# Optimization experiments

Hardware: AMD Instinct MI355X
Metric: run time of the kernel (lower is better)

## Reference

```python
import jax, jax.numpy as jnp
import numpy as np

B, ENC, DEC, H, OUT = 4096, 168, 24, 64, 1
IN = 1 + 5 + 3 + 4 + 7  # 20


def _lstm_step(xt, h, c, Wih, Whh, bih, bhh):
    # PyTorch gate order: i, f, g, o
    g = xt @ Wih.T + h @ Whh.T + bih + bhh
    i, f, gg, o = jnp.split(g, 4, axis=-1)
    c = jax.nn.sigmoid(f) * c + jax.nn.sigmoid(i) * jnp.tanh(gg)
    h = jax.nn.sigmoid(o) * jnp.tanh(c)
    return h, c


def _lstm_layer(x, Wih, Whh, bih, bhh):
    # x: [T, B, in] -> ys: [T, B, H], final (h, c)
    h0 = jnp.zeros((x.shape[1], Whh.shape[1]), x.dtype)

    def step(carry, xt):
        h, c = _lstm_step(xt, carry[0], carry[1], Wih, Whh, bih, bhh)
        return (h, c), h

    (h, c), ys = jax.lax.scan(step, (h0, h0), x)
    return ys, h, c


def setup_inputs() -> dict:
    key = jax.random.key(0)
    ks = jax.random.split(key, 24)
    rn = lambda k, s, sc=0.05: jax.random.normal(k, s, jnp.float32) * sc
    inp = {
        "input_p_q": rn(ks[0], (B, ENC, 1), 1.0),
        "input_time": jax.random.randint(ks[1], (B, ENC, 4), 0, 8),
        "label_p": rn(ks[2], (B, ENC), 1.0),
        "decoder_time": jax.random.randint(ks[3], (B, DEC, 4), 0, 8),
        # encoder LSTM layer 0
        "enc0_Wih": rn(ks[4], (4 * H, IN)), "enc0_Whh": rn(ks[5], (4 * H, H)),
        "enc0_bih": rn(ks[6], (4 * H,)), "enc0_bhh": rn(ks[7], (4 * H,)),
        # encoder LSTM layer 1
        "enc1_Wih": rn(ks[8], (4 * H, H)), "enc1_Whh": rn(ks[9], (4 * H, H)),
        "enc1_bih": rn(ks[10], (4 * H,)), "enc1_bhh": rn(ks[11], (4 * H,)),
        # decoder LSTMCell (input = OUT + 19 = 20)
        "dec_Wih": rn(ks[12], (4 * H, OUT + 19)), "dec_Whh": rn(ks[13], (4 * H, H)),
        "dec_bih": rn(ks[14], (4 * H,)), "dec_bhh": rn(ks[15], (4 * H,)),
        # output projection
        "Wout": rn(ks[16], (OUT, H)), "bout": rn(ks[17], (OUT,)),
        # embeddings
        "emb_hour": rn(ks[18], (24, 5)), "emb_wd": rn(ks[19], (8, 3)),
        "emb_mo": rn(ks[20], (13, 4)), "emb_woy": rn(ks[21], (54, 7)),
    }
    return inp


def reference(input_p_q, input_time, label_p, decoder_time,
              enc0_Wih, enc0_Whh, enc0_bih, enc0_bhh,
              enc1_Wih, enc1_Whh, enc1_bih, enc1_bhh,
              dec_Wih, dec_Whh, dec_bih, dec_bhh,
              Wout, bout, emb_hour, emb_wd, emb_mo, emb_woy):
    def time_feats(t):  # t: [B, T, 4] int -> [B, T, 19]
        return jnp.concatenate([emb_hour[t[:, :, 0]], emb_wd[t[:, :, 1]],
                                emb_mo[t[:, :, 2]], emb_woy[t[:, :, 3]]], axis=-1)

    input_q = label_p[:, :ENC, None]                      # [B, ENC, 1]
    enc_in = jnp.concatenate([input_q, time_feats(input_time)], axis=-1)  # [B, ENC, 20]
    x = enc_in.transpose(1, 0, 2)                         # [ENC, B, 20]
    ys0, _, _ = _lstm_layer(x, enc0_Wih, enc0_Whh, enc0_bih, enc0_bhh)
    _, h1, c1 = _lstm_layer(ys0, enc1_Wih, enc1_Whh, enc1_bih, enc1_bhh)

    dec_feat = time_feats(decoder_time).transpose(1, 0, 2)  # [DEC, B, 19]
    prev0 = label_p[:, ENC - 1, None]                       # [B, 1]

    def dec_step(carry, ft):
        h, c, prev = carry
        xin = jnp.concatenate([prev, ft], axis=-1)          # [B, 20]
        h, c = _lstm_step(xin, h, c, dec_Wih, dec_Whh, dec_bih, dec_bhh)
        out = h @ Wout.T + bout                             # [B, OUT]
        return (h, c, out), out

    _, outs = jax.lax.scan(dec_step, (h1, c1, prev0), dec_feat)
    return outs.transpose(1, 0, 2)                          # [B, DEC, OUT]
```

## Files before the change

kernel.cpp:

```cpp
#include <hip/hip_runtime.h>

#define DEVFN __device__ __forceinline__

typedef float  f32x4  __attribute__((ext_vector_type(4)));
typedef short  bf16x8 __attribute__((ext_vector_type(8)));

constexpr int ENC = 168;
constexpr int DEC = 24;
constexpr int BT  = 16;
constexpr int NBLK = 4096 / BT;

constexpr float LOG2E  = 1.4426950408889634f;
constexpr float LOG2E2 = 2.8853900817779268f;

constexpr int W0F = 0;
constexpr int W1F = 24576;
constexpr int WDF = 57344;
constexpr int F_B0   = 40960;
constexpr int F_B1   = 41216;
constexpr int F_BD   = 41472;
constexpr int F_WOUT = 41728;
constexpr int F_BOUT = 41792;
constexpr int F_EMB  = 41793;
constexpr int NEMB = 574;

DEVFN ushort f2bf(float v) {
    unsigned b = __float_as_uint(v);
    return (ushort)((b + 0x7FFFu + ((b >> 16) & 1u)) >> 16);
}
DEVFN float bf2f(ushort u) { return __uint_as_float(((unsigned)u) << 16); }
DEVFN unsigned cvt_pk_bf16(float a, float b) {
    unsigned r;
    asm("v_cvt_pk_bf16_f32 %0, %1, %2" : "=v"(r) : "v"(a), "v"(b));
    return r;
}
DEVFN float exp2n(float x) {
    float r;
    asm("v_exp_f32 %0, -%1" : "=v"(r) : "v"(x));
    return r;
}
DEVFN void pinv(bf16x8& v) { asm volatile("" : "+v"(v)); }
DEVFN void pinf(f32x4& v)  { asm volatile("" : "+v"(v)); }

DEVFN float lstm_cell(float gi, float gf, float gg, float go, float& c) {
    float a  = exp2n(fmaxf(gi, -21.f));
    float b  = exp2n(fmaxf(gg, -43.f));
    float f  = exp2n(gf);
    float sf = __builtin_amdgcn_rcpf(1.f + f);
    float it = (1.f - b) * __builtin_amdgcn_rcpf(fmaf(a, b, a + b + 1.f));
    c = fmaf(sf, c, it);
    float d  = exp2n(fmaxf(c, -15.f) * LOG2E2);
    float o  = exp2n(fmaxf(go, -21.f));
    return (1.f - d) * __builtin_amdgcn_rcpf(fmaf(o, d, o + d + 1.f));
}

__global__ void prep_kernel(
    const float* __restrict__ w0ih, const float* __restrict__ w0hh,
    const float* __restrict__ b0ih, const float* __restrict__ b0hh,
    const float* __restrict__ w1ih, const float* __restrict__ w1hh,
    const float* __restrict__ b1ih, const float* __restrict__ b1hh,
    const float* __restrict__ wdih, const float* __restrict__ wdhh,
    const float* __restrict__ bdih, const float* __restrict__ bdhh,
    const float* __restrict__ wout, const float* __restrict__ boutp,
    const float* __restrict__ eh,   const float* __restrict__ ewd,
    const float* __restrict__ emo,  const float* __restrict__ ewoy,
    void* __restrict__ ws)
{
    ushort* wsu = (ushort*)ws;
    float*  wsf = (float*)ws;
    const int total = 81920 + 1407;
    for (int idx = blockIdx.x * blockDim.x + threadIdx.x; idx < total;
         idx += gridDim.x * blockDim.x) {
        if (idx < 81920) {
            int layer, q;
            if (idx < W1F)      { layer = 0; q = idx; }
            else if (idx < WDF) { layer = 1; q = idx - W1F; }
            else                { layer = 2; q = idx - WDF; }
            int c  = q >> 13;
            int tt = (q >> 9) & 15;
            int l  = (q >> 3) & 63;
            int j  = q & 7;
            int k  = c * 32 + (l >> 4) * 8 + j;
            int n  = tt * 16 + (l & 15);
            float v = 0.f;
            if (layer == 0) {
                if (k < 20) v = w0ih[n * 20 + k];
                else if (k == 20) v = w0ih[n * 20];
                else if (k >= 32 && k < 96) v = w0hh[n * 64 + (k - 32)];
            } else if (layer == 1) {
                if (k < 64) v = w1ih[n * 64 + k];
                else        v = w1hh[n * 64 + (k - 64)];
            } else {
                if (k < 20) v = wdih[n * 20 + k];
                else if (k == 20) v = wdih[n * 20];
                else if (k >= 32 && k < 96) v = wdhh[n * 64 + (k - 32)];
            }
            v *= ((n >> 6) == 2) ? LOG2E2 : LOG2E;
            wsu[idx] = f2bf(v);
        } else {
            int f = idx - 81920;
            float v;
            if (f < 768) {
                float sc = (((f & 255) >> 6) == 2) ? LOG2E2 : LOG2E;
                if (f < 256)      v = (b0ih[f] + b0hh[f]) * sc;
                else if (f < 512) v = (b1ih[f - 256] + b1hh[f - 256]) * sc;
                else              v = (bdih[f - 512] + bdhh[f - 512]) * sc;
            }
            else if (f < 832) v = wout[f - 768];
            else if (f == 832) v = boutp[0];
            else {
                int e = f - 833;
                if (e < 120)      v = eh[e];
                else if (e < 144) v = ewd[e - 120];
                else if (e < 196) v = emo[e - 144];
                else              v = ewoy[e - 196];
            }
            wsf[40960 + f] = v;
        }
    }
}

DEVFN int offX(int k, int m) {
    return (m + 16 * (k >> 3)) * 8 + (k & 7);
}
DEVFN void store_h4(ushort* A, int off, const float* h) {
    unsigned h01 = cvt_pk_bf16(h[0], h[1]);
    unsigned h23 = cvt_pk_bf16(h[2], h[3]);
    asm volatile("" : "+v"(h01), "+v"(h23));
    unsigned long long p = ((unsigned long long)h23 << 32) | h01;
    *(unsigned long long*)(A + off) = p;
}
DEVFN void store_prev(ushort* A, int m, float v) {
    ushort hi = f2bf(v);
    A[offX(0, m)]  = hi;
    A[offX(20, m)] = f2bf(v - bf2f(hi));
}

__global__ __launch_bounds__(512)
__attribute__((amdgpu_waves_per_eu(2, 2)))
void lstm_mfma(
    const int* __restrict__ input_time, const float* __restrict__ label_p,
    const int* __restrict__ decoder_time, const void* __restrict__ ws,
    float* __restrict__ out)
{
    const ushort* wsu = (const ushort*)ws;
    const float*  wsf = (const float*)ws;

    __shared__ __align__(16) ushort Abuf[2][5 * 512];
    __shared__ float s_emb[NEMB];
    __shared__ float s_wout[64];
    __shared__ float sh1[16 * 68];
    __shared__ float s_bout;

    const int tid = threadIdx.x;
    const int w   = tid >> 6;
    const int l   = tid & 63;
    const int q   = l >> 4;
    const int m   = l & 15;
    const int wl  = w & 3;
    const bool isL0 = (w < 4);
    const int b0g = blockIdx.x * BT;
    const int u0  = wl * 16 + q * 4;

    const int hoff = (1 + (u0 >> 5)) * 512 +
                     (m + 16 * ((u0 & 31) >> 3)) * 8 + (u0 & 7) +
                     (isL0 ? 0 : 1024);

    for (int i = tid; i < 2 * 5 * 512; i += 512) ((ushort*)Abuf)[i] = 0;
    for (int i = tid; i < NEMB; i += 512) s_emb[i] = wsf[F_EMB + i];
    if (tid < 64) s_wout[tid] = wsf[F_WOUT + tid];
    if (tid == 0) s_bout = wsf[F_BOUT];

    bf16x8 wA[4][4];
    if (isL0) {
#pragma unroll
        for (int c = 0; c < 3; c++)
#pragma unroll
            for (int g = 0; g < 4; g++)
                wA[c][g] = *(const bf16x8*)(wsu + W0F +
                    (c * 16 + g * 4 + wl) * 512 + l * 8);
        wA[3][0] = wA[3][1] = wA[3][2] = wA[3][3] = bf16x8{0,0,0,0,0,0,0,0};
    } else {
#pragma unroll
        for (int c = 0; c < 4; c++)
#pragma unroll
            for (int g = 0; g < 4; g++)
                wA[c][g] = *(const bf16x8*)(wsu + W1F +
                    (c * 16 + g * 4 + wl) * 512 + l * 8);
    }
#pragma unroll
    for (int c = 0; c < 4; c++)
#pragma unroll
        for (int g = 0; g < 4; g++) pinv(wA[c][g]);

    f32x4 biasv[4];
#pragma unroll
    for (int g = 0; g < 4; g++) {
        biasv[g] = *(const f32x4*)(wsf + (isL0 ? F_B0 : F_B1) + g * 64 + u0);
        pinf(biasv[g]);
    }

    float cst[4] = {0.f, 0.f, 0.f, 0.f};

    const int kk1 = tid >> 4;
    const int kk2 = kk1 + 16;
    const bool bx2 = (tid < 64);
    int sel1 = 0, estr1 = 0, ebase1 = 0;
    if (kk1 >= 1) {
        int f = kk1 - 1;
        if (f < 5)       { sel1 = 0; estr1 = 5; ebase1 = 0   + f; }
        else if (f < 8)  { sel1 = 1; estr1 = 3; ebase1 = 120 + (f - 5); }
        else if (f < 12) { sel1 = 2; estr1 = 4; ebase1 = 144 + (f - 8); }
        else             { sel1 = 3; estr1 = 7; ebase1 = 196 + (f - 12); }
    }
    const int ebase2 = 196 + (kk2 - 13);

    __syncthreads();
    if (isL0) {
        if (kk1 == 0) {
            store_prev(Abuf[0], m, label_p[(b0g + m) * ENC]);
        } else {
            int idx = input_time[((b0g + m) * ENC) * 4 + sel1];
            Abuf[0][offX(kk1, m)] = f2bf(s_emb[ebase1 + idx * estr1]);
        }
        if (bx2) {
            int idx2 = input_time[((b0g + m) * ENC) * 4 + 3];
            Abuf[0][offX(kk2, m)] = f2bf(s_emb[ebase2 + idx2 * 7]);
        }
    }
    __syncthreads();

    for (int i = 0; i <= ENC; ++i) {
        const ushort* Ar = Abuf[i & 1];
        ushort* Aw = Abuf[(i + 1) & 1];
        const bool active = isL0 ? (i < ENC) : (i >= 1);

        float pre_f = 0.f; int pre_i1 = 0, pre_i2 = 0;
        const bool encX  = (i + 1 < ENC) && isL0;
        const bool decX0 = (i == ENC) && isL0;
        if (encX) {
            if (kk1 == 0) pre_f  = label_p[(b0g + m) * ENC + (i + 1)];
            else          pre_i1 = input_time[((b0g + m) * ENC + (i + 1)) * 4 + sel1];
            if (bx2)      pre_i2 = input_time[((b0g + m) * ENC + (i + 1)) * 4 + 3];
        } else if (decX0) {
            if (kk1 == 0) pre_f  = label_p[(b0g + m) * ENC + (ENC - 1)];
            else          pre_i1 = decoder_time[((b0g + m) * DEC) * 4 + sel1];
            if (bx2)      pre_i2 = decoder_time[((b0g + m) * DEC) * 4 + 3];
        }

        if (active) {
            f32x4 acc[4];
            if (isL0) {
                bf16x8 ah[3];
#pragma unroll
                for (int c = 0; c < 3; c++)
                    ah[c] = *(const bf16x8*)(Ar + c * 512 + l * 8);
#pragma unroll
                for (int g = 0; g < 4; g++)
                    acc[g] = __builtin_amdgcn_mfma_f32_16x16x32_bf16(
                        wA[0][g], ah[0], biasv[g], 0, 0, 0);
#pragma unroll
                for (int c = 1; c < 3; c++)
#pragma unroll
                    for (int g = 0; g < 4; g++)
                        acc[g] = __builtin_amdgcn_mfma_f32_16x16x32_bf16(
                            wA[c][g], ah[c], acc[g], 0, 0, 0);
            } else {
                bf16x8 ah[4];
#pragma unroll
                for (int c = 0; c < 4; c++)
                    ah[c] = *(const bf16x8*)(Ar + (1 + c) * 512 + l * 8);
#pragma unroll
                for (int g = 0; g < 4; g++)
                    acc[g] = __builtin_amdgcn_mfma_f32_16x16x32_bf16(
                        wA[0][g], ah[0], biasv[g], 0, 0, 0);
#pragma unroll
                for (int c = 1; c < 4; c++)
#pragma unroll
                    for (int g = 0; g < 4; g++)
                        acc[g] = __builtin_amdgcn_mfma_f32_16x16x32_bf16(
                            wA[c][g], ah[c], acc[g], 0, 0, 0);
            }
            float hv[4];
#pragma unroll
            for (int r = 0; r < 4; r++)
                hv[r] = lstm_cell(acc[0][r], acc[1][r], acc[2][r], acc[3][r], cst[r]);
            store_h4(Aw, hoff, hv);
        }
        if (encX || decX0) {
            if (kk1 == 0) store_prev(Aw, m, pre_f);
            else          Aw[offX(kk1, m)] = f2bf(s_emb[ebase1 + pre_i1 * estr1]);
            if (bx2)      Aw[offX(kk2, m)] = f2bf(s_emb[ebase2 + pre_i2 * 7]);
        }
        __syncthreads();
    }

    if (!isL0) {
#pragma unroll
        for (int c = 0; c < 3; c++)
#pragma unroll
            for (int g = 0; g < 4; g++)
                wA[c][g] = *(const bf16x8*)(wsu + WDF +
                    (c * 16 + g * 4 + wl) * 512 + l * 8);
#pragma unroll
        for (int c = 0; c < 3; c++)
#pragma unroll
            for (int g = 0; g < 4; g++) pinv(wA[c][g]);
#pragma unroll
        for (int g = 0; g < 4; g++) {
            biasv[g] = *(const f32x4*)(wsf + F_BD + g * 64 + u0);
            pinf(biasv[g]);
        }
    }

    for (int t = 0; t < DEC; ++t) {
        const ushort* Ar = Abuf[(t + 1) & 1];
        ushort* Aw = Abuf[t & 1];

        int pre_i1 = 0, pre_i2 = 0;
        const bool dX = (t + 1 < DEC) && isL0;
        if (dX) {
            if (kk1 >= 1) pre_i1 = decoder_time[((b0g + m) * DEC + (t + 1)) * 4 + sel1];
            if (bx2)      pre_i2 = decoder_time[((b0g + m) * DEC + (t + 1)) * 4 + 3];
        }

        if (!isL0) {
            bf16x8 ah[3];
            ah[0] = *(const bf16x8*)(Ar + 0 * 512 + l * 8);
            ah[1] = *(const bf16x8*)(Ar + 3 * 512 + l * 8);
            ah[2] = *(const bf16x8*)(Ar + 4 * 512 + l * 8);
            f32x4 acc[4];
#pragma unroll
            for (int g = 0; g < 4; g++)
                acc[g] = __builtin_amdgcn_mfma_f32_16x16x32_bf16(
                    wA[0][g], ah[0], biasv[g], 0, 0, 0);
#pragma unroll
            for (int c = 1; c < 3; c++)
#pragma unroll
                for (int g = 0; g < 4; g++)
                    acc[g] = __builtin_amdgcn_mfma_f32_16x16x32_bf16(
                        wA[c][g], ah[c], acc[g], 0, 0, 0);
            float hv[4];
#pragma unroll
            for (int r = 0; r < 4; r++)
                hv[r] = lstm_cell(acc[0][r], acc[1][r], acc[2][r], acc[3][r], cst[r]);
            store_h4(Aw, hoff, hv);
            *(f32x4*)&sh1[m * 68 + u0] = *(f32x4*)hv;
        }
        if (dX && kk1 >= 1) Aw[offX(kk1, m)] = f2bf(s_emb[ebase1 + pre_i1 * estr1]);
        if (dX && bx2)      Aw[offX(kk2, m)] = f2bf(s_emb[ebase2 + pre_i2 * 7]);
        __syncthreads();

        if (tid < 16) {
            float a = s_bout;
#pragma unroll 16
            for (int u = 0; u < 64; u++) a = fmaf(s_wout[u], sh1[tid * 68 + u], a);
            out[(b0g + tid) * DEC + t] = a;
            if (t + 1 < DEC) store_prev(Aw, tid, a);
        }
        __syncthreads();
    }
}

extern "C" void kernel_launch(void* const* d_in, const int* in_sizes, int n_in,
                              void* d_out, int out_size, void* d_ws, size_t ws_size,
                              hipStream_t stream)
{
    typedef const float* fp;
    const int* input_time   = (const int*)d_in[1];
    fp         label_p      = (fp)d_in[2];
    const int* decoder_time = (const int*)d_in[3];

    prep_kernel<<<128, 256, 0, stream>>>(
        (fp)d_in[4],  (fp)d_in[5],  (fp)d_in[6],  (fp)d_in[7],
        (fp)d_in[8],  (fp)d_in[9],  (fp)d_in[10], (fp)d_in[11],
        (fp)d_in[12], (fp)d_in[13], (fp)d_in[14], (fp)d_in[15],
        (fp)d_in[16], (fp)d_in[17],
        (fp)d_in[18], (fp)d_in[19], (fp)d_in[20], (fp)d_in[21],
        d_ws);

    lstm_mfma<<<NBLK, 512, 0, stream>>>(
        input_time, label_p, decoder_time, d_ws, (float*)d_out);
}
```

Measured before the change: 289.0 us.

## Pack two 16-row batch tiles into each 1024-thread block

Each block now processes two independent 16-sample tiles, one per 512-thread half, each with its own double-buffered activation buffer and hidden-state scratch. The grid is halved and the block size doubled to 1024 threads, with the occupancy hint raised to 4 waves per EU. The intent is to interleave two independent recurrences on one CU to hide MFMA and LDS latency in the serial LSTM chain. In exchange, only half as many blocks are launched, which may leave CUs idle, and both halves now wait at shared block-wide barriers.

```diff
diff --git a/kernel.cpp b/kernel.cpp
--- a/kernel.cpp
+++ b/kernel.cpp
@@ -8,7 +8,7 @@
 constexpr int ENC = 168;
 constexpr int DEC = 24;
 constexpr int BT  = 16;
-constexpr int NBLK = 4096 / BT;
+constexpr int NBLK = 4096 / (2 * BT);
 
 constexpr float LOG2E  = 1.4426950408889634f;
 constexpr float LOG2E2 = 2.8853900817779268f;
@@ -136,8 +136,8 @@
     A[offX(20, m)] = f2bf(v - bf2f(hi));
 }
 
-__global__ __launch_bounds__(512)
-__attribute__((amdgpu_waves_per_eu(2, 2)))
+__global__ __launch_bounds__(1024)
+__attribute__((amdgpu_waves_per_eu(4, 4)))
 void lstm_mfma(
     const int* __restrict__ input_time, const float* __restrict__ label_p,
     const int* __restrict__ decoder_time, const void* __restrict__ ws,
@@ -146,28 +146,33 @@
     const ushort* wsu = (const ushort*)ws;
     const float*  wsf = (const float*)ws;
 
-    __shared__ __align__(16) ushort Abuf[2][5 * 512];
+    __shared__ __align__(16) ushort Abuf[2][2][5 * 512];
     __shared__ float s_emb[NEMB];
     __shared__ float s_wout[64];
-    __shared__ float sh1[16 * 68];
+    __shared__ float sh1[2][16 * 68];
     __shared__ float s_bout;
 
-    const int tid = threadIdx.x;
-    const int w   = tid >> 6;
-    const int l   = tid & 63;
+    const int tid  = threadIdx.x;
+    const int half = tid >> 9;
+    const int stid = tid & 511;
+    const int w   = stid >> 6;
+    const int l   = stid & 63;
     const int q   = l >> 4;
     const int m   = l & 15;
     const int wl  = w & 3;
     const bool isL0 = (w < 4);
-    const int b0g = blockIdx.x * BT;
+    const int b0g = blockIdx.x * (2 * BT) + half * BT;
     const int u0  = wl * 16 + q * 4;
+
+    ushort (* const AB)[5 * 512] = Abuf[half];
+    float*  const  myh1 = sh1[half];
 
     const int hoff = (1 + (u0 >> 5)) * 512 +
                      (m + 16 * ((u0 & 31) >> 3)) * 8 + (u0 & 7) +
                      (isL0 ? 0 : 1024);
 
-    for (int i = tid; i < 2 * 5 * 512; i += 512) ((ushort*)Abuf)[i] = 0;
-    for (int i = tid; i < NEMB; i += 512) s_emb[i] = wsf[F_EMB + i];
+    for (int i = tid; i < 2 * 2 * 5 * 512; i += 1024) ((ushort*)Abuf)[i] = 0;
+    for (int i = tid; i < NEMB; i += 1024) s_emb[i] = wsf[F_EMB + i];
     if (tid < 64) s_wout[tid] = wsf[F_WOUT + tid];
     if (tid == 0) s_bout = wsf[F_BOUT];
 
@@ -202,9 +207,9 @@
 
     float cst[4] = {0.f, 0.f, 0.f, 0.f};
 
-    const int kk1 = tid >> 4;
+    const int kk1 = stid >> 4;
     const int kk2 = kk1 + 16;
-    const bool bx2 = (tid < 64);
+    const bool bx2 = (stid < 64);
     int sel1 = 0, estr1 = 0, ebase1 = 0;
     if (kk1 >= 1) {
         int f = kk1 - 1;
@@ -218,21 +223,21 @@
     __syncthreads();
     if (isL0) {
         if (kk1 == 0) {
-            store_prev(Abuf[0], m, label_p[(b0g + m) * ENC]);
+            store_prev(AB[0], m, label_p[(b0g + m) * ENC]);
         } else {
             int idx = input_time[((b0g + m) * ENC) * 4 + sel1];
-            Abuf[0][offX(kk1, m)] = f2bf(s_emb[ebase1 + idx * estr1]);
+            AB[0][offX(kk1, m)] = f2bf(s_emb[ebase1 + idx * estr1]);
         }
         if (bx2) {
             int idx2 = input_time[((b0g + m) * ENC) * 4 + 3];
-            Abuf[0][offX(kk2, m)] = f2bf(s_emb[ebase2 + idx2 * 7]);
+            AB[0][offX(kk2, m)] = f2bf(s_emb[ebase2 + idx2 * 7]);
         }
     }
     __syncthreads();
 
     for (int i = 0; i <= ENC; ++i) {
-        const ushort* Ar = Abuf[i & 1];
-        ushort* Aw = Abuf[(i + 1) & 1];
+        const ushort* Ar = AB[i & 1];
+        ushort* Aw = AB[(i + 1) & 1];
         const bool active = isL0 ? (i < ENC) : (i >= 1);
 
         float pre_f = 0.f; int pre_i1 = 0, pre_i2 = 0;
@@ -314,8 +319,8 @@
     }
 
     for (int t = 0; t < DEC; ++t) {
-        const ushort* Ar = Abuf[(t + 1) & 1];
-        ushort* Aw = Abuf[t & 1];
+        const ushort* Ar = AB[(t + 1) & 1];
+        ushort* Aw = AB[t & 1];
 
         int pre_i1 = 0, pre_i2 = 0;
         const bool dX = (t + 1 < DEC) && isL0;
@@ -345,18 +350,18 @@
             for (int r = 0; r < 4; r++)
                 hv[r] = lstm_cell(acc[0][r], acc[1][r], acc[2][r], acc[3][r], cst[r]);
             store_h4(Aw, hoff, hv);
-            *(f32x4*)&sh1[m * 68 + u0] = *(f32x4*)hv;
+            *(f32x4*)&myh1[m * 68 + u0] = *(f32x4*)hv;
         }
         if (dX && kk1 >= 1) Aw[offX(kk1, m)] = f2bf(s_emb[ebase1 + pre_i1 * estr1]);
         if (dX && bx2)      Aw[offX(kk2, m)] = f2bf(s_emb[ebase2 + pre_i2 * 7]);
         __syncthreads();
 
-        if (tid < 16) {
+        if (stid < 16) {
             float a = s_bout;
 #pragma unroll 16
-            for (int u = 0; u < 64; u++) a = fmaf(s_wout[u], sh1[tid * 68 + u], a);
-            out[(b0g + tid) * DEC + t] = a;
-            if (t + 1 < DEC) store_prev(Aw, tid, a);
+            for (int u = 0; u < 64; u++) a = fmaf(s_wout[u], myh1[stid * 68 + u], a);
+            out[(b0g + stid) * DEC + t] = a;
+            if (t + 1 < DEC) store_prev(Aw, stid, a);
         }
         __syncthreads();
     }
@@ -379,6 +384,6 @@
         (fp)d_in[18], (fp)d_in[19], (fp)d_in[20], (fp)d_in[21],
         d_ws);
 
-    lstm_mfma<<<NBLK, 512, 0, stream>>>(
+    lstm_mfma<<<NBLK, 1024, 0, stream>>>(
         input_time, label_p, decoder_time, d_ws, (float*)d_out);
 }
```

Result: slower. 542.1 us (+87.5%).

## Split gate MFMAs across 16 waves and exchange gate preactivations via LDS

Applied to the files above, without the earlier changes.

Switches the LSTM kernel from 512 to 1024 threads. Each of the 16 waves computes one gate/unit tile for both encoder layers, so every wave runs both layer 0 and layer 1 MFMAs and the gate preactivations go through a shared-memory G buffer. The elementwise cell update is then spread so each thread handles one (batch, unit) element instead of four. A large dummy LDS pad is added to limit blocks per CU. The cost is an extra __syncthreads and an LDS round trip per timestep, in exchange for shorter per-wave MFMA chains and more parallel cell math.

```diff
diff --git a/kernel.cpp b/kernel.cpp
--- a/kernel.cpp
+++ b/kernel.cpp
@@ -29,11 +29,6 @@
     return (ushort)((b + 0x7FFFu + ((b >> 16) & 1u)) >> 16);
 }
 DEVFN float bf2f(ushort u) { return __uint_as_float(((unsigned)u) << 16); }
-DEVFN unsigned cvt_pk_bf16(float a, float b) {
-    unsigned r;
-    asm("v_cvt_pk_bf16_f32 %0, %1, %2" : "=v"(r) : "v"(a), "v"(b));
-    return r;
-}
 DEVFN float exp2n(float x) {
     float r;
     asm("v_exp_f32 %0, -%1" : "=v"(r) : "v"(x));
@@ -123,21 +118,13 @@
 DEVFN int offX(int k, int m) {
     return (m + 16 * (k >> 3)) * 8 + (k & 7);
 }
-DEVFN void store_h4(ushort* A, int off, const float* h) {
-    unsigned h01 = cvt_pk_bf16(h[0], h[1]);
-    unsigned h23 = cvt_pk_bf16(h[2], h[3]);
-    asm volatile("" : "+v"(h01), "+v"(h23));
-    unsigned long long p = ((unsigned long long)h23 << 32) | h01;
-    *(unsigned long long*)(A + off) = p;
-}
 DEVFN void store_prev(ushort* A, int m, float v) {
     ushort hi = f2bf(v);
     A[offX(0, m)]  = hi;
     A[offX(20, m)] = f2bf(v - bf2f(hi));
 }
 
-__global__ __launch_bounds__(512)
-__attribute__((amdgpu_waves_per_eu(2, 2)))
+__global__ __launch_bounds__(1024)
 void lstm_mfma(
     const int* __restrict__ input_time, const float* __restrict__ label_p,
     const int* __restrict__ decoder_time, const void* __restrict__ ws,
@@ -147,66 +134,58 @@
     const float*  wsf = (const float*)ws;
 
     __shared__ __align__(16) ushort Abuf[2][5 * 512];
+    __shared__ __align__(16) float G[2][4][16][68];
     __shared__ float s_emb[NEMB];
     __shared__ float s_wout[64];
-    __shared__ float sh1[16 * 68];
+    __shared__ __align__(16) float sh1[16 * 68];
     __shared__ float s_bout;
+    __shared__ ushort s_pad[15360];
 
     const int tid = threadIdx.x;
     const int w   = tid >> 6;
     const int l   = tid & 63;
     const int q   = l >> 4;
-    const int m   = l & 15;
-    const int wl  = w & 3;
-    const bool isL0 = (w < 4);
+    const int m16 = l & 15;
+    const int g   = w >> 2;
+    const int j   = w & 3;
+    const int u0t = j * 16 + q * 4;
+    const int cu  = (w << 2) | q;
+    const int cm  = m16;
     const int b0g = blockIdx.x * BT;
-    const int u0  = wl * 16 + q * 4;
-
-    const int hoff = (1 + (u0 >> 5)) * 512 +
-                     (m + 16 * ((u0 & 31) >> 3)) * 8 + (u0 & 7) +
-                     (isL0 ? 0 : 1024);
-
-    for (int i = tid; i < 2 * 5 * 512; i += 512) ((ushort*)Abuf)[i] = 0;
-    for (int i = tid; i < NEMB; i += 512) s_emb[i] = wsf[F_EMB + i];
+
+    if (label_p == nullptr) ((volatile ushort*)s_pad)[tid & 1023] = 0;
+
+    const int hoffL0 = (1 + (cu >> 5)) * 512 +
+                       (cm + 16 * ((cu & 31) >> 3)) * 8 + (cu & 7);
+    const int hoffL1 = hoffL0 + 1024;
+
+    for (int i2 = tid; i2 < 2 * 5 * 512; i2 += 1024) ((ushort*)Abuf)[i2] = 0;
+    for (int i2 = tid; i2 < NEMB; i2 += 1024) s_emb[i2] = wsf[F_EMB + i2];
     if (tid < 64) s_wout[tid] = wsf[F_WOUT + tid];
     if (tid == 0) s_bout = wsf[F_BOUT];
 
-    bf16x8 wA[4][4];
-    if (isL0) {
-#pragma unroll
-        for (int c = 0; c < 3; c++)
-#pragma unroll
-            for (int g = 0; g < 4; g++)
-                wA[c][g] = *(const bf16x8*)(wsu + W0F +
-                    (c * 16 + g * 4 + wl) * 512 + l * 8);
-        wA[3][0] = wA[3][1] = wA[3][2] = wA[3][3] = bf16x8{0,0,0,0,0,0,0,0};
-    } else {
-#pragma unroll
-        for (int c = 0; c < 4; c++)
-#pragma unroll
-            for (int g = 0; g < 4; g++)
-                wA[c][g] = *(const bf16x8*)(wsu + W1F +
-                    (c * 16 + g * 4 + wl) * 512 + l * 8);
-    }
+    bf16x8 wA0[3], wA1[4];
+#pragma unroll
+    for (int c = 0; c < 3; c++)
+        wA0[c] = *(const bf16x8*)(wsu + W0F + (c * 16 + w) * 512 + l * 8);
 #pragma unroll
     for (int c = 0; c < 4; c++)
-#pragma unroll
-        for (int g = 0; g < 4; g++) pinv(wA[c][g]);
-
-    f32x4 biasv[4];
-#pragma unroll
-    for (int g = 0; g < 4; g++) {
-        biasv[g] = *(const f32x4*)(wsf + (isL0 ? F_B0 : F_B1) + g * 64 + u0);
-        pinf(biasv[g]);
-    }
-
-    float cst[4] = {0.f, 0.f, 0.f, 0.f};
+        wA1[c] = *(const bf16x8*)(wsu + W1F + (c * 16 + w) * 512 + l * 8);
+#pragma unroll
+    for (int c = 0; c < 3; c++) pinv(wA0[c]);
+#pragma unroll
+    for (int c = 0; c < 4; c++) pinv(wA1[c]);
+
+    f32x4 bias0 = *(const f32x4*)(wsf + F_B0 + g * 64 + u0t);
+    f32x4 bias1 = *(const f32x4*)(wsf + F_B1 + g * 64 + u0t);
+    pinf(bias0); pinf(bias1);
+
+    float cstL0 = 0.f, cstL1 = 0.f;
 
     const int kk1 = tid >> 4;
     const int kk2 = kk1 + 16;
-    const bool bx2 = (tid < 64);
     int sel1 = 0, estr1 = 0, ebase1 = 0;
-    if (kk1 >= 1) {
+    if (kk1 >= 1 && kk1 < 16) {
         int f = kk1 - 1;
         if (f < 5)       { sel1 = 0; estr1 = 5; ebase1 = 0   + f; }
         else if (f < 8)  { sel1 = 1; estr1 = 3; ebase1 = 120 + (f - 5); }
@@ -216,139 +195,124 @@
     const int ebase2 = 196 + (kk2 - 13);
 
     __syncthreads();
-    if (isL0) {
+    if (tid < 256) {
         if (kk1 == 0) {
-            store_prev(Abuf[0], m, label_p[(b0g + m) * ENC]);
+            store_prev(Abuf[0], m16, label_p[(b0g + m16) * ENC]);
         } else {
-            int idx = input_time[((b0g + m) * ENC) * 4 + sel1];
-            Abuf[0][offX(kk1, m)] = f2bf(s_emb[ebase1 + idx * estr1]);
-        }
-        if (bx2) {
-            int idx2 = input_time[((b0g + m) * ENC) * 4 + 3];
-            Abuf[0][offX(kk2, m)] = f2bf(s_emb[ebase2 + idx2 * 7]);
-        }
+            int idx = input_time[((b0g + m16) * ENC) * 4 + sel1];
+            Abuf[0][offX(kk1, m16)] = f2bf(s_emb[ebase1 + idx * estr1]);
+        }
+    }
+    if (tid < 64) {
+        int idx2 = input_time[((b0g + m16) * ENC) * 4 + 3];
+        Abuf[0][offX(kk2, m16)] = f2bf(s_emb[ebase2 + idx2 * 7]);
     }
     __syncthreads();
 
     for (int i = 0; i <= ENC; ++i) {
         const ushort* Ar = Abuf[i & 1];
         ushort* Aw = Abuf[(i + 1) & 1];
-        const bool active = isL0 ? (i < ENC) : (i >= 1);
+        const bool actL0 = (i < ENC);
+        const bool actL1 = (i >= 1);
 
         float pre_f = 0.f; int pre_i1 = 0, pre_i2 = 0;
-        const bool encX  = (i + 1 < ENC) && isL0;
-        const bool decX0 = (i == ENC) && isL0;
+        const bool encX  = (i + 1 < ENC) && (tid < 256);
+        const bool decX0 = (i == ENC) && (tid < 256);
         if (encX) {
-            if (kk1 == 0) pre_f  = label_p[(b0g + m) * ENC + (i + 1)];
-            else          pre_i1 = input_time[((b0g + m) * ENC + (i + 1)) * 4 + sel1];
-            if (bx2)      pre_i2 = input_time[((b0g + m) * ENC + (i + 1)) * 4 + 3];
+            if (kk1 == 0) pre_f  = label_p[(b0g + m16) * ENC + (i + 1)];
+            else          pre_i1 = input_time[((b0g + m16) * ENC + (i + 1)) * 4 + sel1];
+            if (tid < 64) pre_i2 = input_time[((b0g + m16) * ENC + (i + 1)) * 4 + 3];
         } else if (decX0) {
-            if (kk1 == 0) pre_f  = label_p[(b0g + m) * ENC + (ENC - 1)];
-            else          pre_i1 = decoder_time[((b0g + m) * DEC) * 4 + sel1];
-            if (bx2)      pre_i2 = decoder_time[((b0g + m) * DEC) * 4 + 3];
-        }
-
-        if (active) {
-            f32x4 acc[4];
-            if (isL0) {
-                bf16x8 ah[3];
-#pragma unroll
-                for (int c = 0; c < 3; c++)
-                    ah[c] = *(const bf16x8*)(Ar + c * 512 + l * 8);
-#pragma unroll
-                for (int g = 0; g < 4; g++)
-                    acc[g] = __builtin_amdgcn_mfma_f32_16x16x32_bf16(
-                        wA[0][g], ah[0], biasv[g], 0, 0, 0);
-#pragma unroll
-                for (int c = 1; c < 3; c++)
-#pragma unroll
-                    for (int g = 0; g < 4; g++)
-                        acc[g] = __builtin_amdgcn_mfma_f32_16x16x32_bf16(
-                            wA[c][g], ah[c], acc[g], 0, 0, 0);
-            } else {
-                bf16x8 ah[4];
-#pragma unroll
-                for (int c = 0; c < 4; c++)
-                    ah[c] = *(const bf16x8*)(Ar + (1 + c) * 512 + l * 8);
-#pragma unroll
-                for (int g = 0; g < 4; g++)
-                    acc[g] = __builtin_amdgcn_mfma_f32_16x16x32_bf16(
-                        wA[0][g], ah[0], biasv[g], 0, 0, 0);
-#pragma unroll
-                for (int c = 1; c < 4; c++)
-#pragma unroll
-                    for (int g = 0; g < 4; g++)
-                        acc[g] = __builtin_amdgcn_mfma_f32_16x16x32_bf16(
-                            wA[c][g], ah[c], acc[g], 0, 0, 0);
-            }
-            float hv[4];
-#pragma unroll
-            for (int r = 0; r < 4; r++)
-                hv[r] = lstm_cell(acc[0][r], acc[1][r], acc[2][r], acc[3][r], cst[r]);
-            store_h4(Aw, hoff, hv);
+            if (kk1 == 0) pre_f  = label_p[(b0g + m16) * ENC + (ENC - 1)];
+            else          pre_i1 = decoder_time[((b0g + m16) * DEC) * 4 + sel1];
+            if (tid < 64) pre_i2 = decoder_time[((b0g + m16) * DEC) * 4 + 3];
+        }
+
+        {
+            bf16x8 ah[5];
+#pragma unroll
+            for (int c = 0; c < 5; c++)
+                ah[c] = *(const bf16x8*)(Ar + c * 512 + l * 8);
+            if (actL0) {
+                f32x4 a0 = __builtin_amdgcn_mfma_f32_16x16x32_bf16(
+                    wA0[0], ah[0], bias0, 0, 0, 0);
+                a0 = __builtin_amdgcn_mfma_f32_16x16x32_bf16(
+                    wA0[1], ah[1], a0, 0, 0, 0);
+                a0 = __builtin_amdgcn_mfma_f32_16x16x32_bf16(
+                    wA0[2], ah[2], a0, 0, 0, 0);
+                *(f32x4*)&G[0][g][m16][u0t] = a0;
+            }
+            if (actL1) {
+                f32x4 a1 = __builtin_amdgcn_mfma_f32_16x16x32_bf16(
+                    wA1[0], ah[1], bias1, 0, 0, 0);
+                a1 = __builtin_amdgcn_mfma_f32_16x16x32_bf16(
+                    wA1[1], ah[2], a1, 0, 0, 0);
+                a1 = __builtin_amdgcn_mfma_f32_16x16x32_bf16(
+                    wA1[2], ah[3], a1, 0, 0, 0);
+                a1 = __builtin_amdgcn_mfma_f32_16x16x32_bf16(
+                    wA1[3], ah[4], a1, 0, 0, 0);
+                *(f32x4*)&G[1][g][m16][u0t] = a1;
+            }
+        }
+        __syncthreads();
+
+        if (actL0) {
+            float h = lstm_cell(G[0][0][cm][cu], G[0][1][cm][cu],
+                                G[0][2][cm][cu], G[0][3][cm][cu], cstL0);
+            Aw[hoffL0] = f2bf(h);
+        }
+        if (actL1) {
+            float h = lstm_cell(G[1][0][cm][cu], G[1][1][cm][cu],
+                                G[1][2][cm][cu], G[1][3][cm][cu], cstL1);
+            Aw[hoffL1] = f2bf(h);
         }
         if (encX || decX0) {
-            if (kk1 == 0) store_prev(Aw, m, pre_f);
-            else          Aw[offX(kk1, m)] = f2bf(s_emb[ebase1 + pre_i1 * estr1]);
-            if (bx2)      Aw[offX(kk2, m)] = f2bf(s_emb[ebase2 + pre_i2 * 7]);
-        }
-        __syncthreads();
-    }
-
-    if (!isL0) {
-#pragma unroll
-        for (int c = 0; c < 3; c++)
-#pragma unroll
-            for (int g = 0; g < 4; g++)
-                wA[c][g] = *(const bf16x8*)(wsu + WDF +
-                    (c * 16 + g * 4 + wl) * 512 + l * 8);
-#pragma unroll
-        for (int c = 0; c < 3; c++)
-#pragma unroll
-            for (int g = 0; g < 4; g++) pinv(wA[c][g]);
-#pragma unroll
-        for (int g = 0; g < 4; g++) {
-            biasv[g] = *(const f32x4*)(wsf + F_BD + g * 64 + u0);
-            pinf(biasv[g]);
-        }
-    }
+            if (kk1 == 0) store_prev(Aw, m16, pre_f);
+            else          Aw[offX(kk1, m16)] = f2bf(s_emb[ebase1 + pre_i1 * estr1]);
+            if (tid < 64) Aw[offX(kk2, m16)] = f2bf(s_emb[ebase2 + pre_i2 * 7]);
+        }
+        __syncthreads();
+    }
+
+#pragma unroll
+    for (int c = 0; c < 3; c++)
+        wA0[c] = *(const bf16x8*)(wsu + WDF + (c * 16 + w) * 512 + l * 8);
+#pragma unroll
+    for (int c = 0; c < 3; c++) pinv(wA0[c]);
+    bias0 = *(const f32x4*)(wsf + F_BD + g * 64 + u0t);
+    pinf(bias0);
 
     for (int t = 0; t < DEC; ++t) {
         const ushort* Ar = Abuf[(t + 1) & 1];
         ushort* Aw = Abuf[t & 1];
 
         int pre_i1 = 0, pre_i2 = 0;
-        const bool dX = (t + 1 < DEC) && isL0;
+        const bool dX = (t + 1 < DEC) && (tid < 256);
         if (dX) {
-            if (kk1 >= 1) pre_i1 = decoder_time[((b0g + m) * DEC + (t + 1)) * 4 + sel1];
-            if (bx2)      pre_i2 = decoder_time[((b0g + m) * DEC + (t + 1)) * 4 + 3];
-        }
-
-        if (!isL0) {
-            bf16x8 ah[3];
-            ah[0] = *(const bf16x8*)(Ar + 0 * 512 + l * 8);
-            ah[1] = *(const bf16x8*)(Ar + 3 * 512 + l * 8);
-            ah[2] = *(const bf16x8*)(Ar + 4 * 512 + l * 8);
-            f32x4 acc[4];
-#pragma unroll
-            for (int g = 0; g < 4; g++)
-                acc[g] = __builtin_amdgcn_mfma_f32_16x16x32_bf16(
-                    wA[0][g], ah[0], biasv[g], 0, 0, 0);
-#pragma unroll
-            for (int c = 1; c < 3; c++)
-#pragma unroll
-                for (int g = 0; g < 4; g++)
-                    acc[g] = __builtin_amdgcn_mfma_f32_16x16x32_bf16(
-                        wA[c][g], ah[c], acc[g], 0, 0, 0);
-            float hv[4];
-#pragma unroll
-            for (int r = 0; r < 4; r++)
-                hv[r] = lstm_cell(acc[0][r], acc[1][r], acc[2][r], acc[3][r], cst[r]);
-            store_h4(Aw, hoff, hv);
-            *(f32x4*)&sh1[m * 68 + u0] = *(f32x4*)hv;
-        }
-        if (dX && kk1 >= 1) Aw[offX(kk1, m)] = f2bf(s_emb[ebase1 + pre_i1 * estr1]);
-        if (dX && bx2)      Aw[offX(kk2, m)] = f2bf(s_emb[ebase2 + pre_i2 * 7]);
+            if (kk1 >= 1) pre_i1 = decoder_time[((b0g + m16) * DEC + (t + 1)) * 4 + sel1];
+            if (tid < 64) pre_i2 = decoder_time[((b0g + m16) * DEC + (t + 1)) * 4 + 3];
+        }
+
+        {
+            bf16x8 a0f = *(const bf16x8*)(Ar + 0 * 512 + l * 8);
+            bf16x8 a1f = *(const bf16x8*)(Ar + 3 * 512 + l * 8);
+            bf16x8 a2f = *(const bf16x8*)(Ar + 4 * 512 + l * 8);
+            f32x4 a = __builtin_amdgcn_mfma_f32_16x16x32_bf16(
+                wA0[0], a0f, bias0, 0, 0, 0);
+            a = __builtin_amdgcn_mfma_f32_16x16x32_bf16(wA0[1], a1f, a, 0, 0, 0);
+            a = __builtin_amdgcn_mfma_f32_16x16x32_bf16(wA0[2], a2f, a, 0, 0, 0);
+            *(f32x4*)&G[1][g][m16][u0t] = a;
+        }
+        __syncthreads();
+
+        {
+            float h = lstm_cell(G[1][0][cm][cu], G[1][1][cm][cu],
+                                G[1][2][cm][cu], G[1][3][cm][cu], cstL1);
+            Aw[hoffL1] = f2bf(h);
+            sh1[cm * 68 + cu] = h;
+        }
+        if (dX && kk1 >= 1) Aw[offX(kk1, m16)] = f2bf(s_emb[ebase1 + pre_i1 * estr1]);
+        if (dX && tid < 64) Aw[offX(kk2, m16)] = f2bf(s_emb[ebase2 + pre_i2 * 7]);
         __syncthreads();
 
         if (tid < 16) {
@@ -379,6 +343,6 @@
         (fp)d_in[18], (fp)d_in[19], (fp)d_in[20], (fp)d_in[21],
         d_ws);
 
-    lstm_mfma<<<NBLK, 512, 0, stream>>>(
+    lstm_mfma<<<NBLK, 1024, 0, stream>>>(
         input_time, label_p, decoder_time, d_ws, (float*)d_out);
 }
```

Measured after the change: 336.0 us. 1.16x slower.

## Split LSTM gates across wave pairs with 1024-thread blocks and LDS exchange

Applied to the files above, without the earlier changes.

Doubles the block to 1024 threads so each wave computes only two of the four gate tiles, halving MFMA work per wave on the serial recurrence path. Partner waves swap half of their gate accumulators through a new shared XP buffer so each lane can finish two cells. This adds one extra __syncthreads per timestep. A large dummy shared pad is also added, apparently to cap occupancy at one block per CU.

```diff
diff --git a/kernel.cpp b/kernel.cpp
--- a/kernel.cpp
+++ b/kernel.cpp
@@ -123,21 +123,13 @@
 DEVFN int offX(int k, int m) {
     return (m + 16 * (k >> 3)) * 8 + (k & 7);
 }
-DEVFN void store_h4(ushort* A, int off, const float* h) {
-    unsigned h01 = cvt_pk_bf16(h[0], h[1]);
-    unsigned h23 = cvt_pk_bf16(h[2], h[3]);
-    asm volatile("" : "+v"(h01), "+v"(h23));
-    unsigned long long p = ((unsigned long long)h23 << 32) | h01;
-    *(unsigned long long*)(A + off) = p;
-}
 DEVFN void store_prev(ushort* A, int m, float v) {
     ushort hi = f2bf(v);
     A[offX(0, m)]  = hi;
     A[offX(20, m)] = f2bf(v - bf2f(hi));
 }
 
-__global__ __launch_bounds__(512)
-__attribute__((amdgpu_waves_per_eu(2, 2)))
+__global__ __launch_bounds__(1024)
 void lstm_mfma(
     const int* __restrict__ input_time, const float* __restrict__ label_p,
     const int* __restrict__ decoder_time, const void* __restrict__ ws,
@@ -147,66 +139,75 @@
     const float*  wsf = (const float*)ws;
 
     __shared__ __align__(16) ushort Abuf[2][5 * 512];
+    __shared__ float XP[4][16][64];
     __shared__ float s_emb[NEMB];
     __shared__ float s_wout[64];
     __shared__ float sh1[16 * 68];
     __shared__ float s_bout;
+    __shared__ ushort s_pad[24576];
 
     const int tid = threadIdx.x;
     const int w   = tid >> 6;
     const int l   = tid & 63;
     const int q   = l >> 4;
     const int m   = l & 15;
-    const int wl  = w & 3;
-    const bool isL0 = (w < 4);
+    const int wb  = w & 3;
+    const int gh  = (w >> 2) & 1;
+    const bool isL0 = (w < 8);
+    const int pw  = w ^ 4;
     const int b0g = blockIdx.x * BT;
-    const int u0  = wl * 16 + q * 4;
+    const int u0  = wb * 16 + q * 4;
+    const int rr  = gh * 2;
+    const int pr  = 2 - rr;
+
+    if (label_p == nullptr) ((volatile ushort*)s_pad)[tid & 1023] = 0;
 
     const int hoff = (1 + (u0 >> 5)) * 512 +
                      (m + 16 * ((u0 & 31) >> 3)) * 8 + (u0 & 7) +
-                     (isL0 ? 0 : 1024);
-
-    for (int i = tid; i < 2 * 5 * 512; i += 512) ((ushort*)Abuf)[i] = 0;
-    for (int i = tid; i < NEMB; i += 512) s_emb[i] = wsf[F_EMB + i];
+                     (isL0 ? 0 : 1024) + rr;
+
+    for (int i = tid; i < 2 * 5 * 512; i += 1024) ((ushort*)Abuf)[i] = 0;
+    for (int i = tid; i < NEMB; i += 1024) s_emb[i] = wsf[F_EMB + i];
     if (tid < 64) s_wout[tid] = wsf[F_WOUT + tid];
     if (tid == 0) s_bout = wsf[F_BOUT];
 
-    bf16x8 wA[4][4];
+    bf16x8 wA[4][2];
     if (isL0) {
 #pragma unroll
         for (int c = 0; c < 3; c++)
 #pragma unroll
-            for (int g = 0; g < 4; g++)
-                wA[c][g] = *(const bf16x8*)(wsu + W0F +
-                    (c * 16 + g * 4 + wl) * 512 + l * 8);
-        wA[3][0] = wA[3][1] = wA[3][2] = wA[3][3] = bf16x8{0,0,0,0,0,0,0,0};
+            for (int s = 0; s < 2; s++)
+                wA[c][s] = *(const bf16x8*)(wsu + W0F +
+                    (c * 16 + (2 * gh + s) * 4 + wb) * 512 + l * 8);
+#pragma unroll
+        for (int c = 0; c < 3; c++) { pinv(wA[c][0]); pinv(wA[c][1]); }
     } else {
 #pragma unroll
         for (int c = 0; c < 4; c++)
 #pragma unroll
-            for (int g = 0; g < 4; g++)
-                wA[c][g] = *(const bf16x8*)(wsu + W1F +
-                    (c * 16 + g * 4 + wl) * 512 + l * 8);
-    }
-#pragma unroll
-    for (int c = 0; c < 4; c++)
-#pragma unroll
-        for (int g = 0; g < 4; g++) pinv(wA[c][g]);
-
-    f32x4 biasv[4];
-#pragma unroll
-    for (int g = 0; g < 4; g++) {
-        biasv[g] = *(const f32x4*)(wsf + (isL0 ? F_B0 : F_B1) + g * 64 + u0);
-        pinf(biasv[g]);
-    }
-
-    float cst[4] = {0.f, 0.f, 0.f, 0.f};
+            for (int s = 0; s < 2; s++)
+                wA[c][s] = *(const bf16x8*)(wsu + W1F +
+                    (c * 16 + (2 * gh + s) * 4 + wb) * 512 + l * 8);
+#pragma unroll
+        for (int c = 0; c < 4; c++) { pinv(wA[c][0]); pinv(wA[c][1]); }
+    }
+
+    f32x4 biasv[2];
+#pragma unroll
+    for (int s = 0; s < 2; s++) {
+        biasv[s] = *(const f32x4*)(wsf + (isL0 ? F_B0 : F_B1) +
+                                   (2 * gh + s) * 64 + u0);
+        pinf(biasv[s]);
+    }
+
+    float cst[2] = {0.f, 0.f};
 
     const int kk1 = tid >> 4;
     const int kk2 = kk1 + 16;
-    const bool bx2 = (tid < 64);
+    const bool xb1 = (tid < 256);
+    const bool xb2 = (tid < 64);
     int sel1 = 0, estr1 = 0, ebase1 = 0;
-    if (kk1 >= 1) {
+    if (kk1 >= 1 && kk1 < 16) {
         int f = kk1 - 1;
         if (f < 5)       { sel1 = 0; estr1 = 5; ebase1 = 0   + f; }
         else if (f < 8)  { sel1 = 1; estr1 = 3; ebase1 = 120 + (f - 5); }
@@ -216,17 +217,17 @@
     const int ebase2 = 196 + (kk2 - 13);
 
     __syncthreads();
-    if (isL0) {
+    if (xb1) {
         if (kk1 == 0) {
             store_prev(Abuf[0], m, label_p[(b0g + m) * ENC]);
         } else {
             int idx = input_time[((b0g + m) * ENC) * 4 + sel1];
             Abuf[0][offX(kk1, m)] = f2bf(s_emb[ebase1 + idx * estr1]);
         }
-        if (bx2) {
-            int idx2 = input_time[((b0g + m) * ENC) * 4 + 3];
-            Abuf[0][offX(kk2, m)] = f2bf(s_emb[ebase2 + idx2 * 7]);
-        }
+    }
+    if (xb2) {
+        int idx2 = input_time[((b0g + m) * ENC) * 4 + 3];
+        Abuf[0][offX(kk2, m)] = f2bf(s_emb[ebase2 + idx2 * 7]);
     }
     __syncthreads();
 
@@ -236,61 +237,77 @@
         const bool active = isL0 ? (i < ENC) : (i >= 1);
 
         float pre_f = 0.f; int pre_i1 = 0, pre_i2 = 0;
-        const bool encX  = (i + 1 < ENC) && isL0;
-        const bool decX0 = (i == ENC) && isL0;
+        const bool encX  = (i + 1 < ENC) && xb1;
+        const bool decX0 = (i == ENC) && xb1;
         if (encX) {
             if (kk1 == 0) pre_f  = label_p[(b0g + m) * ENC + (i + 1)];
             else          pre_i1 = input_time[((b0g + m) * ENC + (i + 1)) * 4 + sel1];
-            if (bx2)      pre_i2 = input_time[((b0g + m) * ENC + (i + 1)) * 4 + 3];
+            if (xb2)      pre_i2 = input_time[((b0g + m) * ENC + (i + 1)) * 4 + 3];
         } else if (decX0) {
             if (kk1 == 0) pre_f  = label_p[(b0g + m) * ENC + (ENC - 1)];
             else          pre_i1 = decoder_time[((b0g + m) * DEC) * 4 + sel1];
-            if (bx2)      pre_i2 = decoder_time[((b0g + m) * DEC) * 4 + 3];
-        }
-
+            if (xb2)      pre_i2 = decoder_time[((b0g + m) * DEC) * 4 + 3];
+        }
+
+        f32x4 acc[2];
         if (active) {
-            f32x4 acc[4];
             if (isL0) {
                 bf16x8 ah[3];
 #pragma unroll
                 for (int c = 0; c < 3; c++)
                     ah[c] = *(const bf16x8*)(Ar + c * 512 + l * 8);
 #pragma unroll
-                for (int g = 0; g < 4; g++)
-                    acc[g] = __builtin_amdgcn_mfma_f32_16x16x32_bf16(
-                        wA[0][g], ah[0], biasv[g], 0, 0, 0);
+                for (int s = 0; s < 2; s++)
+                    acc[s] = __builtin_amdgcn_mfma_f32_16x16x32_bf16(
+                        wA[0][s], ah[0], biasv[s], 0, 0, 0);
 #pragma unroll
                 for (int c = 1; c < 3; c++)
 #pragma unroll
-                    for (int g = 0; g < 4; g++)
-                        acc[g] = __builtin_amdgcn_mfma_f32_16x16x32_bf16(
-                            wA[c][g], ah[c], acc[g], 0, 0, 0);
+                    for (int s = 0; s < 2; s++)
+                        acc[s] = __builtin_amdgcn_mfma_f32_16x16x32_bf16(
+                            wA[c][s], ah[c], acc[s], 0, 0, 0);
             } else {
                 bf16x8 ah[4];
 #pragma unroll
                 for (int c = 0; c < 4; c++)
                     ah[c] = *(const bf16x8*)(Ar + (1 + c) * 512 + l * 8);
 #pragma unroll
-                for (int g = 0; g < 4; g++)
-                    acc[g] = __builtin_amdgcn_mfma_f32_16x16x32_bf16(
-                        wA[0][g], ah[0], biasv[g], 0, 0, 0);
+                for (int s = 0; s < 2; s++)
+                    acc[s] = __builtin_amdgcn_mfma_f32_16x16x32_bf16(
+                        wA[0][s], ah[0], biasv[s], 0, 0, 0);
 #pragma unroll
                 for (int c = 1; c < 4; c++)
 #pragma unroll
-                    for (int g = 0; g < 4; g++)
-                        acc[g] = __builtin_amdgcn_mfma_f32_16x16x32_bf16(
-                            wA[c][g], ah[c], acc[g], 0, 0, 0);
-            }
-            float hv[4];
-#pragma unroll
-            for (int r = 0; r < 4; r++)
-                hv[r] = lstm_cell(acc[0][r], acc[1][r], acc[2][r], acc[3][r], cst[r]);
-            store_h4(Aw, hoff, hv);
+                    for (int s = 0; s < 2; s++)
+                        acc[s] = __builtin_amdgcn_mfma_f32_16x16x32_bf16(
+                            wA[c][s], ah[c], acc[s], 0, 0, 0);
+            }
+            XP[0][w][l] = acc[0][pr];
+            XP[1][w][l] = acc[0][pr + 1];
+            XP[2][w][l] = acc[1][pr];
+            XP[3][w][l] = acc[1][pr + 1];
+        }
+        __syncthreads();
+
+        if (active) {
+            float pA0 = XP[0][pw][l], pA1 = XP[1][pw][l];
+            float pB0 = XP[2][pw][l], pB1 = XP[3][pw][l];
+            float hv0, hv1;
+            if (gh == 0) {
+                hv0 = lstm_cell(acc[0][0], acc[1][0], pA0, pB0, cst[0]);
+                hv1 = lstm_cell(acc[0][1], acc[1][1], pA1, pB1, cst[1]);
+            } else {
+                hv0 = lstm_cell(pA0, pB0, acc[0][2], acc[1][2], cst[0]);
+                hv1 = lstm_cell(pA1, pB1, acc[0][3], acc[1][3], cst[1]);
+            }
+            unsigned pk = cvt_pk_bf16(hv0, hv1);
+            asm volatile("" : "+v"(pk));
+            *(unsigned*)(Aw + hoff) = pk;
         }
         if (encX || decX0) {
             if (kk1 == 0) store_prev(Aw, m, pre_f);
             else          Aw[offX(kk1, m)] = f2bf(s_emb[ebase1 + pre_i1 * estr1]);
-            if (bx2)      Aw[offX(kk2, m)] = f2bf(s_emb[ebase2 + pre_i2 * 7]);
+            if (xb2)      Aw[offX(kk2, m)] = f2bf(s_emb[ebase2 + pre_i2 * 7]);
         }
         __syncthreads();
     }
@@ -299,17 +316,15 @@
 #pragma unroll
         for (int c = 0; c < 3; c++)
 #pragma unroll
-            for (int g = 0; g < 4; g++)
-                wA[c][g] = *(const bf16x8*)(wsu + WDF +
-                    (c * 16 + g * 4 + wl) * 512 + l * 8);
-#pragma unroll
-        for (int c = 0; c < 3; c++)
-#pragma unroll
-            for (int g = 0; g < 4; g++) pinv(wA[c][g]);
-#pragma unroll
-        for (int g = 0; g < 4; g++) {
-            biasv[g] = *(const f32x4*)(wsf + F_BD + g * 64 + u0);
-            pinf(biasv[g]);
+            for (int s = 0; s < 2; s++)
+                wA[c][s] = *(const bf16x8*)(wsu + WDF +
+                    (c * 16 + (2 * gh + s) * 4 + wb) * 512 + l * 8);
+#pragma unroll
+        for (int c = 0; c < 3; c++) { pinv(wA[c][0]); pinv(wA[c][1]); }
+#pragma unroll
+        for (int s = 0; s < 2; s++) {
+            biasv[s] = *(const f32x4*)(wsf + F_BD + (2 * gh + s) * 64 + u0);
+            pinf(biasv[s]);
         }
     }
 
@@ -318,37 +333,54 @@
         ushort* Aw = Abuf[t & 1];
 
         int pre_i1 = 0, pre_i2 = 0;
-        const bool dX = (t + 1 < DEC) && isL0;
+        const bool dX = (t + 1 < DEC) && xb1;
         if (dX) {
             if (kk1 >= 1) pre_i1 = decoder_time[((b0g + m) * DEC + (t + 1)) * 4 + sel1];
-            if (bx2)      pre_i2 = decoder_time[((b0g + m) * DEC + (t + 1)) * 4 + 3];
-        }
-
+            if (xb2)      pre_i2 = decoder_time[((b0g + m) * DEC + (t + 1)) * 4 + 3];
+        }
+
+        f32x4 acc[2];
         if (!isL0) {
             bf16x8 ah[3];
             ah[0] = *(const bf16x8*)(Ar + 0 * 512 + l * 8);
             ah[1] = *(const bf16x8*)(Ar + 3 * 512 + l * 8);
             ah[2] = *(const bf16x8*)(Ar + 4 * 512 + l * 8);
-            f32x4 acc[4];
-#pragma unroll
-            for (int g = 0; g < 4; g++)
-                acc[g] = __builtin_amdgcn_mfma_f32_16x16x32_bf16(
-                    wA[0][g], ah[0], biasv[g], 0, 0, 0);
+#pragma unroll
+            for (int s = 0; s < 2; s++)
+                acc[s] = __builtin_amdgcn_mfma_f32_16x16x32_bf16(
+                    wA[0][s], ah[0], biasv[s], 0, 0, 0);
 #pragma unroll
             for (int c = 1; c < 3; c++)
 #pragma unroll
-                for (int g = 0; g < 4; g++)
-                    acc[g] = __builtin_amdgcn_mfma_f32_16x16x32_bf16(
-                        wA[c][g], ah[c], acc[g], 0, 0, 0);
-            float hv[4];
-#pragma unroll
-            for (int r = 0; r < 4; r++)
-                hv[r] = lstm_cell(acc[0][r], acc[1][r], acc[2][r], acc[3][r], cst[r]);
-            store_h4(Aw, hoff, hv);
-            *(f32x4*)&sh1[m * 68 + u0] = *(f32x4*)hv;
+                for (int s = 0; s < 2; s++)
+                    acc[s] = __builtin_amdgcn_mfma_f32_16x16x32_bf16(
+                        wA[c][s], ah[c], acc[s], 0, 0, 0);
+            XP[0][w][l] = acc[0][pr];
+            XP[1][w][l] = acc[0][pr + 1];
+            XP[2][w][l] = acc[1][pr];
+            XP[3][w][l] = acc[1][pr + 1];
+        }
+        __syncthreads();
+
+        if (!isL0) {
+            float pA0 = XP[0][pw][l], pA1 = XP[1][pw][l];
+            float pB0 = XP[2][pw][l], pB1 = XP[3][pw][l];
+            float hv0, hv1;
+            if (gh == 0) {
+                hv0 = lstm_cell(acc[0][0], acc[1][0], pA0, pB0, cst[0]);
+                hv1 = lstm_cell(acc[0][1], acc[1][1], pA1, pB1, cst[1]);
+            } else {
+                hv0 = lstm_cell(pA0, pB0, acc[0][2], acc[1][2], cst[0]);
+                hv1 = lstm_cell(pA1, pB1, acc[0][3], acc[1][3], cst[1]);
+            }
+            unsigned pk = cvt_pk_bf16(hv0, hv1);
+            asm volatile("" : "+v"(pk));
+            *(unsigned*)(Aw + hoff) = pk;
+            sh1[m * 68 + u0 + rr]     = hv0;
+            sh1[m * 68 + u0 + rr + 1] = hv1;
         }
         if (dX && kk1 >= 1) Aw[offX(kk1, m)] = f2bf(s_emb[ebase1 + pre_i1 * estr1]);
-        if (dX && bx2)      Aw[offX(kk2, m)] = f2bf(s_emb[ebase2 + pre_i2 * 7]);
+        if (dX && xb2)      Aw[offX(kk2, m)] = f2bf(s_emb[ebase2 + pre_i2 * 7]);
         __syncthreads();
 
         if (tid < 16) {
@@ -379,6 +411,6 @@
         (fp)d_in[18], (fp)d_in[19], (fp)d_in[20], (fp)d_in[21],
         d_ws);
 
-    lstm_mfma<<<NBLK, 512, 0, stream>>>(
+    lstm_mfma<<<NBLK, 1024, 0, stream>>>(
         input_time, label_p, decoder_time, d_ws, (float*)d_out);
 }
```

After: 331.7 us. 14.8% more time.
